# Performance work log

Hardware: AMD Instinct MI355X
Metric: run time of the kernel (lower is better)

Reference implementation:

```python
import jax, jax.numpy as jnp
from jax import lax
import numpy as np

# --- constants matching harris_laplace_detector_batch defaults ---
NUM_OCTAVES = 6
INITIAL_SIGMA = 1.4
HARRIS_K = 0.04
THRESHOLD = 0.01

SOBEL_X = jnp.array([[-1., 0., 1.], [-2., 0., 2.], [-1., 0., 1.]], jnp.float32)
SOBEL_Y = SOBEL_X.T
# OpenCV Laplacian kernel for ksize=3
LAP3 = jnp.array([[2., 0., 2.], [0., -8., 0.], [2., 0., 2.]], jnp.float32)


def _conv2d(x, k):
    """Cross-correlate x [N,H,W] with kernel k [kh,kw], reflect-101 padding (cv2 default)."""
    kh, kw = k.shape
    pt, pb = kh // 2, kh - 1 - kh // 2
    pl, pr = kw // 2, kw - 1 - kw // 2
    xp = jnp.pad(x, ((0, 0), (pt, pb), (pl, pr)), mode='reflect')
    out = lax.conv_general_dilated(xp[:, None], k[None, None], (1, 1), 'VALID')
    return out[:, 0]


def _gaussian_blur(x, sigma):
    """Separable Gaussian blur, truncated at ~3 sigma (static kernel size per octave)."""
    r = max(1, int(3.0 * sigma + 0.5))
    t = jnp.arange(-r, r + 1, dtype=jnp.float32)
    g = jnp.exp(-0.5 * (t / sigma) ** 2)
    g = g / g.sum()
    x = _conv2d(x, g[None, :])  # blur rows
    x = _conv2d(x, g[:, None])  # blur cols
    return x


def setup_inputs() -> dict:
    key = jax.random.key(0)
    images = jax.random.uniform(key, (16, 3, 512, 512), dtype=jnp.float32)
    return {"images": images}


def reference(images) -> jnp.ndarray:
    B, C, H, W = images.shape
    x = images.reshape(B * C, H, W)  # treat each channel independently, as the torch loop does

    # cv2.normalize(..., 0, 255, NORM_MINMAX) per channel (continuous analogue of uint8 cast)
    mn = x.min(axis=(1, 2), keepdims=True)
    mx = x.max(axis=(1, 2), keepdims=True)
    gray = (x - mn) / (mx - mn + 1e-12) * 255.0

    # Harris response: Sobel gradients (ksize=3), 2x2 unnormalized box sum (blockSize=2)
    Ix = _conv2d(gray, SOBEL_X)
    Iy = _conv2d(gray, SOBEL_Y)
    box = jnp.ones((2, 2), jnp.float32)
    Sxx = _conv2d(Ix * Ix, box)
    Syy = _conv2d(Iy * Iy, box)
    Sxy = _conv2d(Ix * Iy, box)
    R = Sxx * Syy - Sxy * Sxy - HARRIS_K * (Sxx + Syy) ** 2

    # cv2.dilate with default 3x3 kernel = 3x3 max filter
    Rd = lax.reduce_window(R, -jnp.inf, lax.max, (1, 3, 3), (1, 1, 1), 'SAME')
    mask = (Rd > THRESHOLD * Rd.max(axis=(1, 2), keepdims=True)).astype(jnp.float32)

    # multi-octave |scaled Laplacian| blurred at each sigma, max-combined
    lap_base = _conv2d(gray, LAP3)
    combined = jnp.zeros_like(gray)
    for octave in range(NUM_OCTAVES):
        sigma = INITIAL_SIGMA * (2.0 ** octave)
        lap = jnp.abs(_gaussian_blur(lap_base * sigma, sigma))
        combined = jnp.maximum(combined, mask * lap)

    # max over channels (the torch loop keeps running np.maximum across channels)
    corners = combined.reshape(B, C, H, W).max(axis=1, keepdims=True)  # [B,1,H,W]
    return corners
```

## Files before the change

### kernel.cpp

```cpp
#include <hip/hip_runtime.h>

#define W 512
#define NPX (512*512)
#define NCH 48
#define NBATCH 16

__device__ __forceinline__ int refl(int i) {
    int a = i < 0 ? -i : i;
    int b = 1022 - a;
    return a < b ? a : b;
}
__device__ __forceinline__ unsigned encf(float f) {
    unsigned u = __float_as_uint(f);
    return (u & 0x80000000u) ? ~u : (u | 0x80000000u);
}
__device__ __forceinline__ float decf(unsigned e) {
    unsigned u = (e & 0x80000000u) ? (e & 0x7FFFFFFFu) : ~e;
    return __uint_as_float(u);
}
__device__ __forceinline__ unsigned long long enc64(double d) {
    unsigned long long u = (unsigned long long)__double_as_longlong(d);
    return (u & 0x8000000000000000ULL) ? ~u : (u | 0x8000000000000000ULL);
}
__device__ __forceinline__ double dec64(unsigned long long e) {
    unsigned long long u = (e & 0x8000000000000000ULL) ? (e & 0x7FFFFFFFFFFFFFFFULL) : ~e;
    return __longlong_as_double((long long)u);
}

__global__ void initK(unsigned* minenc, unsigned* maxenc, unsigned long long* rmaxenc) {
    int t = threadIdx.x;
    if (t < NCH) { minenc[t] = 0xFFFFFFFFu; maxenc[t] = 0u; rmaxenc[t] = 0ULL; }
}

__global__ void gaussK(float* gw) {
    int o = blockIdx.x;
    const int rr[6] = {4, 8, 17, 34, 67, 134};
    int r = rr[o];
    float sigma = 1.4f * (float)(1 << o);
    int t = threadIdx.x;
    int n = 2*r + 1;
    float wv = 0.f;
    if (t < n) { float ft = (float)(t - r) / sigma; wv = expf(-0.5f * ft * ft); }
    __shared__ float red[512];
    red[t] = wv; __syncthreads();
    for (int s = 256; s > 0; s >>= 1) { if (t < s) red[t] += red[t + s]; __syncthreads(); }
    float sum = red[0];
    float* g = gw + o*288;
    if (t < 288) g[t] = (t < n) ? wv / sum : 0.f;
}

__global__ void minmaxK(const float4* __restrict__ x4, unsigned* minenc, unsigned* maxenc) {
    int ch = blockIdx.y, chunk = blockIdx.x, t = threadIdx.x;
    size_t base = (size_t)ch*(NPX/4) + (size_t)chunk*8192;
    float mn = 3.4e38f, mx = -3.4e38f;
    for (int i = t; i < 8192; i += 256) {
        float4 v = x4[base + i];
        mn = fminf(mn, fminf(fminf(v.x, v.y), fminf(v.z, v.w)));
        mx = fmaxf(mx, fmaxf(fmaxf(v.x, v.y), fmaxf(v.z, v.w)));
    }
    for (int o = 32; o; o >>= 1) { mn = fminf(mn, __shfl_down(mn, o)); mx = fmaxf(mx, __shfl_down(mx, o)); }
    __shared__ float smn[4], smx[4];
    if ((t & 63) == 0) { smn[t >> 6] = mn; smx[t >> 6] = mx; }
    __syncthreads();
    if (t == 0) {
        for (int i = 1; i < 4; i++) { mn = fminf(mn, smn[i]); mx = fmaxf(mx, smx[i]); }
        atomicMin(&minenc[ch], encf(mn));
        atomicMax(&maxenc[ch], encf(mx));
    }
}

__global__ void scaleK(const unsigned* minenc, const unsigned* maxenc, double* gsd) {
    int t = threadIdx.x;
    if (t >= NCH) return;
    double mn = (double)decf(minenc[t]), mx = (double)decf(maxenc[t]);
    gsd[t] = 255.0 / (mx - mn + 1e-12);
}

__global__ __launch_bounds__(256) void lapRK(const float* __restrict__ x, const double* __restrict__ gsd,
                      float* __restrict__ lap, double* __restrict__ Rb,
                      unsigned long long* __restrict__ rmaxenc) {
    __shared__ float in[36*36];
    __shared__ double Pxx[33*34], Pyy[33*34], Pxy[33*34];
    int ch = blockIdx.z;
    int px0 = blockIdx.x * 32, py0 = blockIdx.y * 32;
    const float* s = x + (size_t)ch*NPX;
    int t = threadIdx.x;
    for (int i = t; i < 36*36; i += 256) {
        int yy = i / 36, xx = i - yy*36;
        in[i] = s[(size_t)refl(py0 - 2 + yy)*W + refl(px0 - 2 + xx)];
    }
    __syncthreads();
    for (int i = t; i < 33*33; i += 256) {
        int ly = i / 33, lx = i - ly*33;
        const float* c = &in[(ly+1)*36 + (lx+1)];
        double v00 = c[-37], v01 = c[-36], v02 = c[-35];
        double v10 = c[-1],                v12 = c[1];
        double v20 = c[35],  v21 = c[36],  v22 = c[37];
        double ix = (v02 - v00) + 2.0*(v12 - v10) + (v22 - v20);
        double iy = (v20 - v00) + 2.0*(v21 - v01) + (v22 - v02);
        Pxx[ly*34+lx] = ix*ix; Pyy[ly*34+lx] = iy*iy; Pxy[ly*34+lx] = ix*iy;
    }
    __syncthreads();
    double sd = gsd[ch], s2 = sd*sd;
    int tx = t & 31, ty0 = (t >> 5) * 4;
    double m = -1e308;
    #pragma unroll
    for (int q = 0; q < 4; q++) {
        int ly = ty0 + q;
        int gy = py0 + ly, gx = px0 + tx;
        int ya = (gy ? gy-1 : 1) - py0 + 1;
        int yb = ly + 1;
        int xa = (gx ? gx-1 : 1) - px0 + 1;
        int xb = tx + 1;
        double Sxx = (Pxx[ya*34+xa] + Pxx[ya*34+xb]) + (Pxx[yb*34+xa] + Pxx[yb*34+xb]);
        double Syy = (Pyy[ya*34+xa] + Pyy[ya*34+xb]) + (Pyy[yb*34+xa] + Pyy[yb*34+xb]);
        double Sxy = (Pxy[ya*34+xa] + Pxy[ya*34+xb]) + (Pxy[yb*34+xa] + Pxy[yb*34+xb]);
        Sxx *= s2; Syy *= s2; Sxy *= s2;
        double tr = Sxx + Syy;
        double R = Sxx*Syy - Sxy*Sxy - 0.04*tr*tr;
        Rb[(size_t)ch*NPX + (size_t)gy*W + gx] = R;
        const float* c = &in[(ly+2)*36 + (tx+2)];
        double l = 2.0*((double)c[-37] + (double)c[-35] + (double)c[35] + (double)c[37]) - 8.0*(double)c[0];
        lap[(size_t)ch*NPX + (size_t)gy*W + gx] = (float)(sd * l);
        m = fmax(m, R);
    }
    for (int o = 32; o; o >>= 1) m = fmax(m, __shfl_down(m, o));
    __shared__ double sred[4];
    if ((t & 63) == 0) sred[t >> 6] = m;
    __syncthreads();
    if (t == 0) {
        for (int i = 1; i < 4; i++) m = fmax(m, sred[i]);
        atomicMax(&rmaxenc[ch], enc64(m));
    }
}

__global__ __launch_bounds__(256) void maskTK(const double* __restrict__ Rb,
                                              const unsigned long long* __restrict__ rmaxenc,
                                              unsigned char* __restrict__ maskb) {
    __shared__ int bt[34*34];
    int ch = blockIdx.z;
    int px0 = blockIdx.x*32, py0 = blockIdx.y*32;
    double thr = 0.01 * dec64(rmaxenc[ch]);
    const double* R = Rb + (size_t)ch*NPX;
    int t = threadIdx.x;
    for (int i = t; i < 34*34; i += 256) {
        int yy = i / 34, xx = i - yy*34;
        int gy = py0 - 1 + yy, gx = px0 - 1 + xx;
        int v = 0;
        if ((unsigned)gy < 512u && (unsigned)gx < 512u) v = (R[(size_t)gy*W + gx] > thr) ? 1 : 0;
        bt[i] = v;
    }
    __syncthreads();
    int tx = t & 31, ty0 = (t >> 5) * 4;
    #pragma unroll
    for (int q = 0; q < 4; q++) {
        int ly = ty0 + q;
        int c = (ly+1)*34 + tx + 1;
        int v = bt[c-35] | bt[c-34] | bt[c-33] | bt[c-1] | bt[c] | bt[c+1] | bt[c+33] | bt[c+34] | bt[c+35];
        maskb[(size_t)ch*NPX + (size_t)(py0+ly)*W + px0 + tx] = (unsigned char)v;
    }
}

__global__ __launch_bounds__(256) void rowblurK(const float* __restrict__ src, float* __restrict__ dst,
                                                const float* __restrict__ gwo, int r, int nc2) {
    __shared__ float ES[8][16][49];
    __shared__ float wl[272];
    int ch = blockIdx.y;
    int row0 = blockIdx.x * 8;
    int t = threadIdx.x;
    int lr = t >> 5, xi = t & 31;
    for (int i = t; i < 272; i += 256) wl[i] = gwo[i];
    const float* s = src + (size_t)ch*NPX + (size_t)(row0 + lr)*W;
    int n = W + 2*r;
    for (int j = xi; j < 784; j += 32) {
        float v = (j < n) ? s[refl(j - r)] : 0.f;
        ES[lr][j & 15][j >> 4] = v;
    }
    __syncthreads();
    float a[16];
    #pragma unroll
    for (int m = 0; m < 16; m++) a[m] = 0.f;
    for (int cc = 0; cc < nc2; ++cc) {
        float wv[16], f[31];
        #pragma unroll
        for (int i = 0; i < 16; i++) wv[i] = wl[16*cc + i];
        #pragma unroll
        for (int j = 0; j < 31; j++) f[j] = ES[lr][j & 15][xi + cc + (j >> 4)];
        #pragma unroll
        for (int m = 0; m < 16; m++) {
            #pragma unroll
            for (int i = 0; i < 16; i++) a[m] = fmaf(wv[i], f[m + i], a[m]);
        }
    }
    float4* d4 = (float4*)(dst + (size_t)ch*NPX + (size_t)(row0 + lr)*W + xi*16);
    d4[0] = make_float4(a[0],  a[1],  a[2],  a[3]);
    d4[1] = make_float4(a[4],  a[5],  a[6],  a[7]);
    d4[2] = make_float4(a[8],  a[9],  a[10], a[11]);
    d4[3] = make_float4(a[12], a[13], a[14], a[15]);
}

template<int RPT, int CHUNK>
__global__ __launch_bounds__(256, (RPT == 4) ? 4 : 2)
void colblurK(const float* __restrict__ T, const unsigned char* __restrict__ maskb,
              float* __restrict__ out, const float* __restrict__ gwo,
              int r, int nchunk, int rowsAlloc, float sigma, int write0) {
    extern __shared__ __align__(16) float tile[];
    float* wl = tile + rowsAlloc*36;
    const int BAND = RPT*32;
    int x0 = blockIdx.x * 32;
    int band0 = blockIdx.y * BAND;
    int b = blockIdx.z;
    int t = threadIdx.x;
    int cg = t & 7, rg = t >> 3;
    int j0 = rg * RPT;
    int rowsData = BAND + 2*r;
    for (int i = t; i < 288; i += 256) wl[i] = gwo[i];
    float4 vm[RPT];
    #pragma unroll
    for (int m = 0; m < RPT; m++) vm[m] = make_float4(0.f, 0.f, 0.f, 0.f);
    for (int c = 0; c < 3; ++c) {
        int ch = b*3 + c;
        __syncthreads();
        const float* src = T + (size_t)ch*NPX;
        for (int ly = rg; ly < rowsAlloc; ly += 32) {
            float4 v = make_float4(0.f, 0.f, 0.f, 0.f);
            if (ly < rowsData) v = *(const float4*)(src + (size_t)refl(band0 - r + ly)*W + x0 + 4*cg);
            *(float4*)(tile + ly*36 + 4*cg) = v;
        }
        __syncthreads();
        const unsigned char* mp = maskb + (size_t)ch*NPX + (size_t)(band0 + j0)*W + x0 + 4*cg;
        unsigned mk = 0;
        #pragma unroll
        for (int m = 0; m < RPT; m++) {
            uchar4 u = *(const uchar4*)(mp + (size_t)m*W);
            mk |= ((u.x ? 1u : 0u) | (u.y ? 2u : 0u) | (u.z ? 4u : 0u) | (u.w ? 8u : 0u)) << (4*m);
        }
        if (__any((int)(mk != 0))) {
            float4 a[RPT];
            #pragma unroll
            for (int m = 0; m < RPT; m++) a[m] = make_float4(0.f, 0.f, 0.f, 0.f);
            const float* tb = tile + j0*36 + 4*cg;
            for (int cc = 0; cc < nchunk; ++cc) {
                const float* tc = tb + CHUNK*cc*36;
                float4 f[RPT + CHUNK - 1];
                #pragma unroll
                for (int j = 0; j < RPT + CHUNK - 1; j++) f[j] = *(const float4*)(tc + j*36);
                float wv[CHUNK];
                #pragma unroll
                for (int q = 0; q < CHUNK/4; q++) {
                    float4 w4 = *(const float4*)(wl + CHUNK*cc + 4*q);
                    wv[4*q] = w4.x; wv[4*q+1] = w4.y; wv[4*q+2] = w4.z; wv[4*q+3] = w4.w;
                }
                #pragma unroll
                for (int m = 0; m < RPT; m++) {
                    #pragma unroll
                    for (int i = 0; i < CHUNK; i++) {
                        a[m].x = fmaf(wv[i], f[m+i].x, a[m].x);
                        a[m].y = fmaf(wv[i], f[m+i].y, a[m].y);
                        a[m].z = fmaf(wv[i], f[m+i].z, a[m].z);
                        a[m].w = fmaf(wv[i], f[m+i].w, a[m].w);
                    }
                }
            }
            #pragma unroll
            for (int m = 0; m < RPT; m++) {
                if (mk & (1u << (4*m+0))) vm[m].x = fmaxf(vm[m].x, sigma*fabsf(a[m].x));
                if (mk & (1u << (4*m+1))) vm[m].y = fmaxf(vm[m].y, sigma*fabsf(a[m].y));
                if (mk & (1u << (4*m+2))) vm[m].z = fmaxf(vm[m].z, sigma*fabsf(a[m].z));
                if (mk & (1u << (4*m+3))) vm[m].w = fmaxf(vm[m].w, sigma*fabsf(a[m].w));
            }
        }
    }
    float* ob = out + (size_t)b*NPX + (size_t)(band0 + j0)*W + x0 + 4*cg;
    #pragma unroll
    for (int m = 0; m < RPT; m++) {
        float4 v = vm[m];
        if (!write0) {
            float4 cur = *(const float4*)(ob + (size_t)m*W);
            v.x = fmaxf(v.x, cur.x); v.y = fmaxf(v.y, cur.y);
            v.z = fmaxf(v.z, cur.z); v.w = fmaxf(v.w, cur.w);
        }
        *(float4*)(ob + (size_t)m*W) = v;
    }
}

extern "C" void kernel_launch(void* const* d_in, const int* in_sizes, int n_in,
                              void* d_out, int out_size, void* d_ws, size_t ws_size,
                              hipStream_t stream) {
    const float* x = (const float*)d_in[0];
    float* out = (float*)d_out;
    char* w = (char*)d_ws;
    unsigned* minenc           = (unsigned*)(w + 1024);
    unsigned* maxenc           = (unsigned*)(w + 1280);
    unsigned long long* rmaxenc= (unsigned long long*)(w + 1536);
    double*  gsd               = (double*)(w + 256);
    float*   gw                = (float*)(w + 2048);
    float*   lap               = (float*)(w + 16384);
    double*  Rb                = (double*)(w + 16384 + 50331648);
    float*   T                 = (float*)Rb;
    unsigned char* maskb       = (unsigned char*)(w + 16384 + 50331648 + 100663296);

    initK<<<1, 64, 0, stream>>>(minenc, maxenc, rmaxenc);
    gaussK<<<6, 512, 0, stream>>>(gw);
    minmaxK<<<dim3(8, 48), 256, 0, stream>>>((const float4*)x, minenc, maxenc);
    scaleK<<<1, 64, 0, stream>>>(minenc, maxenc, gsd);
    lapRK<<<dim3(16, 16, 48), 256, 0, stream>>>(x, gsd, lap, Rb, rmaxenc);
    maskTK<<<dim3(16, 16, 48), 256, 0, stream>>>(Rb, rmaxenc, maskb);

    const int rr[6] = {4, 8, 17, 34, 67, 134};
    for (int o = 0; o < 6; ++o) {
        int r = rr[o];
        int nc16 = (2*r + 1 + 15) / 16;
        float sigma = 1.4f * (float)(1 << o);
        rowblurK<<<dim3(64, 48), 256, 0, stream>>>(lap, T, gw + o*288, r, nc16);
        if (o == 5) {
            int nc = nc16;
            int rowsAlloc = 256 + 16*nc;
            size_t lds = (size_t)(rowsAlloc*36 + 288) * 4;
            colblurK<8,16><<<dim3(16, 2, 16), 256, lds, stream>>>(T, maskb, out, gw + o*288, r, nc, rowsAlloc, sigma, 0);
        } else {
            int nc = (2*r + 1 + 7) / 8;
            int rowsAlloc = 128 + 8*nc;
            size_t lds = (size_t)(rowsAlloc*36 + 288) * 4;
            colblurK<4,8><<<dim3(16, 4, 16), 256, lds, stream>>>(T, maskb, out, gw + o*288, r, nc, rowsAlloc, sigma, o == 0 ? 1 : 0);
        }
    }
}
```

Baseline: 702.8 us.

## Skip blur work for mask-inactive rows and restructure Harris and column blur

Adds a per-channel row-activity bitmap built in the mask kernel and uses it to skip row-blur blocks and column-blur channels whose output is never selected by the mask. The Harris stage now computes Sobel gradients and the 2x2 box sum directly from registers instead of staging products in shared memory. The column blur becomes a single 8-row-per-thread variant with a sliding register window that reuses loaded rows across chunks. This adds atomics, extra launch arguments and larger LDS tiles, and the amount of work skipped depends on how sparse the mask is.

```diff
diff --git a/kernel.cpp b/kernel.cpp
--- a/kernel.cpp
+++ b/kernel.cpp
@@ -27,9 +27,11 @@
     return __longlong_as_double((long long)u);
 }
 
-__global__ void initK(unsigned* minenc, unsigned* maxenc, unsigned long long* rmaxenc) {
+__global__ void initK(unsigned* minenc, unsigned* maxenc, unsigned long long* rmaxenc,
+                      unsigned* rowact) {
     int t = threadIdx.x;
     if (t < NCH) { minenc[t] = 0xFFFFFFFFu; maxenc[t] = 0u; rmaxenc[t] = 0ULL; }
+    for (int i = t; i < NCH*16; i += 1024) rowact[i] = 0u;
 }
 
 __global__ void gaussK(float* gw) {
@@ -80,7 +82,6 @@
                       float* __restrict__ lap, double* __restrict__ Rb,
                       unsigned long long* __restrict__ rmaxenc) {
     __shared__ float in[36*36];
-    __shared__ double Pxx[33*34], Pyy[33*34], Pxy[33*34];
     int ch = blockIdx.z;
     int px0 = blockIdx.x * 32, py0 = blockIdx.y * 32;
     const float* s = x + (size_t)ch*NPX;
@@ -90,31 +91,42 @@
         in[i] = s[(size_t)refl(py0 - 2 + yy)*W + refl(px0 - 2 + xx)];
     }
     __syncthreads();
-    for (int i = t; i < 33*33; i += 256) {
-        int ly = i / 33, lx = i - ly*33;
-        const float* c = &in[(ly+1)*36 + (lx+1)];
-        double v00 = c[-37], v01 = c[-36], v02 = c[-35];
-        double v10 = c[-1],                v12 = c[1];
-        double v20 = c[35],  v21 = c[36],  v22 = c[37];
-        double ix = (v02 - v00) + 2.0*(v12 - v10) + (v22 - v20);
-        double iy = (v20 - v00) + 2.0*(v21 - v01) + (v22 - v02);
-        Pxx[ly*34+lx] = ix*ix; Pyy[ly*34+lx] = iy*iy; Pxy[ly*34+lx] = ix*iy;
-    }
-    __syncthreads();
     double sd = gsd[ch], s2 = sd*sd;
     int tx = t & 31, ty0 = (t >> 5) * 4;
+    int gx = px0 + tx;
+    int cb = gx ? tx : 1;
     double m = -1e308;
     #pragma unroll
     for (int q = 0; q < 4; q++) {
         int ly = ty0 + q;
-        int gy = py0 + ly, gx = px0 + tx;
-        int ya = (gy ? gy-1 : 1) - py0 + 1;
-        int yb = ly + 1;
-        int xa = (gx ? gx-1 : 1) - px0 + 1;
-        int xb = tx + 1;
-        double Sxx = (Pxx[ya*34+xa] + Pxx[ya*34+xb]) + (Pxx[yb*34+xa] + Pxx[yb*34+xb]);
-        double Syy = (Pyy[ya*34+xa] + Pyy[ya*34+xb]) + (Pyy[yb*34+xa] + Pyy[yb*34+xb]);
-        double Sxy = (Pxy[ya*34+xa] + Pxy[ya*34+xb]) + (Pxy[yb*34+xa] + Pxy[yb*34+xb]);
+        int gy = py0 + ly;
+        int rb = gy ? ly : 1;
+        double w[4][4];
+        #pragma unroll
+        for (int j = 0; j < 4; j++) {
+            const float* rp = &in[(rb + j)*36 + cb];
+            w[j][0] = (double)rp[0]; w[j][1] = (double)rp[1];
+            w[j][2] = (double)rp[2]; w[j][3] = (double)rp[3];
+        }
+        double cs1[4], cs2[4], rs[4][2];
+        #pragma unroll
+        for (int c2 = 0; c2 < 4; c2++) {
+            cs1[c2] = w[0][c2] + 2.0*w[1][c2] + w[2][c2];
+            cs2[c2] = w[1][c2] + 2.0*w[2][c2] + w[3][c2];
+        }
+        #pragma unroll
+        for (int j = 0; j < 4; j++) {
+            rs[j][0] = w[j][0] + 2.0*w[j][1] + w[j][2];
+            rs[j][1] = w[j][1] + 2.0*w[j][2] + w[j][3];
+        }
+        double Sxx = 0, Syy = 0, Sxy = 0;
+        {
+            double ix, iy;
+            ix = cs1[2]-cs1[0]; iy = rs[2][0]-rs[0][0]; Sxx += ix*ix; Syy += iy*iy; Sxy += ix*iy;
+            ix = cs1[3]-cs1[1]; iy = rs[2][1]-rs[0][1]; Sxx += ix*ix; Syy += iy*iy; Sxy += ix*iy;
+            ix = cs2[2]-cs2[0]; iy = rs[3][0]-rs[1][0]; Sxx += ix*ix; Syy += iy*iy; Sxy += ix*iy;
+            ix = cs2[3]-cs2[1]; iy = rs[3][1]-rs[1][1]; Sxx += ix*ix; Syy += iy*iy; Sxy += ix*iy;
+        }
         Sxx *= s2; Syy *= s2; Sxy *= s2;
         double tr = Sxx + Syy;
         double R = Sxx*Syy - Sxy*Sxy - 0.04*tr*tr;
@@ -136,13 +148,16 @@
 
 __global__ __launch_bounds__(256) void maskTK(const double* __restrict__ Rb,
                                               const unsigned long long* __restrict__ rmaxenc,
-                                              unsigned char* __restrict__ maskb) {
+                                              unsigned char* __restrict__ maskb,
+                                              unsigned* __restrict__ rowact) {
     __shared__ int bt[34*34];
+    __shared__ unsigned rw;
     int ch = blockIdx.z;
     int px0 = blockIdx.x*32, py0 = blockIdx.y*32;
     double thr = 0.01 * dec64(rmaxenc[ch]);
     const double* R = Rb + (size_t)ch*NPX;
     int t = threadIdx.x;
+    if (t == 0) rw = 0u;
     for (int i = t; i < 34*34; i += 256) {
         int yy = i / 34, xx = i - yy*34;
         int gy = py0 - 1 + yy, gx = px0 - 1 + xx;
@@ -158,16 +173,41 @@
         int c = (ly+1)*34 + tx + 1;
         int v = bt[c-35] | bt[c-34] | bt[c-33] | bt[c-1] | bt[c] | bt[c+1] | bt[c+33] | bt[c+34] | bt[c+35];
         maskb[(size_t)ch*NPX + (size_t)(py0+ly)*W + px0 + tx] = (unsigned char)v;
-    }
+        unsigned long long bal = __ballot(v != 0);
+        int lane = t & 63;
+        if (lane == 0 && (unsigned)bal) atomicOr(&rw, 1u << (ty0 + q));
+        if (lane == 32 && (unsigned)(bal >> 32)) atomicOr(&rw, 1u << (ty0 + q));
+    }
+    __syncthreads();
+    if (t == 0 && rw) atomicOr(&rowact[ch*16 + (py0 >> 5)], rw);
 }
 
 __global__ __launch_bounds__(256) void rowblurK(const float* __restrict__ src, float* __restrict__ dst,
-                                                const float* __restrict__ gwo, int r, int nc2) {
+                                                const float* __restrict__ gwo, int r, int nc2,
+                                                const unsigned* __restrict__ rowact) {
+    int ch = blockIdx.y;
+    int row0 = blockIdx.x * 8;
+    int t = threadIdx.x;
+    {
+        int lo = row0 - r - 7; if (lo < 0) lo = 0;
+        int hi = row0 + 7 + r; if (hi > 511) hi = 511;
+        int w0 = lo >> 5, w1 = hi >> 5;
+        int lane = t & 63;
+        unsigned any = 0;
+        if (lane <= w1 - w0) {
+            int wi = w0 + lane;
+            unsigned word = rowact[ch*16 + wi];
+            int b0 = wi*32;
+            int lo2 = lo > b0 ? lo - b0 : 0;
+            int hi2 = hi < b0 + 31 ? hi - b0 : 31;
+            unsigned mlo = ~0u << lo2;
+            unsigned mhi = (hi2 == 31) ? ~0u : ((1u << (hi2 + 1)) - 1u);
+            any = word & mlo & mhi;
+        }
+        if (!__any((int)(any != 0))) return;
+    }
     __shared__ float ES[8][16][49];
     __shared__ float wl[272];
-    int ch = blockIdx.y;
-    int row0 = blockIdx.x * 8;
-    int t = threadIdx.x;
     int lr = t >> 5, xi = t & 31;
     for (int i = t; i < 272; i += 256) wl[i] = gwo[i];
     const float* s = src + (size_t)ch*NPX + (size_t)(row0 + lr)*W;
@@ -199,28 +239,35 @@
     d4[3] = make_float4(a[12], a[13], a[14], a[15]);
 }
 
-template<int RPT, int CHUNK>
-__global__ __launch_bounds__(256, (RPT == 4) ? 4 : 2)
-void colblurK(const float* __restrict__ T, const unsigned char* __restrict__ maskb,
-              float* __restrict__ out, const float* __restrict__ gwo,
-              int r, int nchunk, int rowsAlloc, float sigma, int write0) {
+__global__ __launch_bounds__(256) void colblurK(const float* __restrict__ T, const unsigned char* __restrict__ maskb,
+                                                float* __restrict__ out, const float* __restrict__ gwo,
+                                                int r, int nchunk, int rowsAlloc, float sigma, int write0) {
     extern __shared__ __align__(16) float tile[];
     float* wl = tile + rowsAlloc*36;
-    const int BAND = RPT*32;
     int x0 = blockIdx.x * 32;
-    int band0 = blockIdx.y * BAND;
+    int band0 = blockIdx.y * 256;
     int b = blockIdx.z;
     int t = threadIdx.x;
     int cg = t & 7, rg = t >> 3;
-    int j0 = rg * RPT;
-    int rowsData = BAND + 2*r;
+    int j0 = rg * 8;
+    int rowsData = 256 + 2*r;
     for (int i = t; i < 288; i += 256) wl[i] = gwo[i];
-    float4 vm[RPT];
-    #pragma unroll
-    for (int m = 0; m < RPT; m++) vm[m] = make_float4(0.f, 0.f, 0.f, 0.f);
+    float4 vm[8];
+    #pragma unroll
+    for (int m = 0; m < 8; m++) vm[m] = make_float4(0.f, 0.f, 0.f, 0.f);
+    int anyAct = 0;
     for (int c = 0; c < 3; ++c) {
         int ch = b*3 + c;
-        __syncthreads();
+        const unsigned char* mp = maskb + (size_t)ch*NPX + (size_t)(band0 + j0)*W + x0 + 4*cg;
+        unsigned mk = 0;
+        #pragma unroll
+        for (int m = 0; m < 8; m++) {
+            uchar4 u = *(const uchar4*)(mp + (size_t)m*W);
+            mk |= ((u.x ? 1u : 0u) | (u.y ? 2u : 0u) | (u.z ? 4u : 0u) | (u.w ? 8u : 0u)) << (4*m);
+        }
+        int act = __syncthreads_or((int)(mk != 0));
+        if (!act) continue;
+        anyAct = 1;
         const float* src = T + (size_t)ch*NPX;
         for (int ly = rg; ly < rowsAlloc; ly += 32) {
             float4 v = make_float4(0.f, 0.f, 0.f, 0.f);
@@ -228,33 +275,31 @@
             *(float4*)(tile + ly*36 + 4*cg) = v;
         }
         __syncthreads();
-        const unsigned char* mp = maskb + (size_t)ch*NPX + (size_t)(band0 + j0)*W + x0 + 4*cg;
-        unsigned mk = 0;
-        #pragma unroll
-        for (int m = 0; m < RPT; m++) {
-            uchar4 u = *(const uchar4*)(mp + (size_t)m*W);
-            mk |= ((u.x ? 1u : 0u) | (u.y ? 2u : 0u) | (u.z ? 4u : 0u) | (u.w ? 8u : 0u)) << (4*m);
-        }
         if (__any((int)(mk != 0))) {
-            float4 a[RPT];
+            float4 a[8];
             #pragma unroll
-            for (int m = 0; m < RPT; m++) a[m] = make_float4(0.f, 0.f, 0.f, 0.f);
+            for (int m = 0; m < 8; m++) a[m] = make_float4(0.f, 0.f, 0.f, 0.f);
             const float* tb = tile + j0*36 + 4*cg;
+            float4 f[15];
+            #pragma unroll
+            for (int j = 0; j < 15; j++) f[j] = *(const float4*)(tb + j*36);
             for (int cc = 0; cc < nchunk; ++cc) {
-                const float* tc = tb + CHUNK*cc*36;
-                float4 f[RPT + CHUNK - 1];
+                if (cc) {
+                    #pragma unroll
+                    for (int j = 0; j < 7; j++) f[j] = f[j+8];
+                    #pragma unroll
+                    for (int j = 7; j < 15; j++) f[j] = *(const float4*)(tb + (8*cc + j)*36);
+                }
+                float wv[8];
                 #pragma unroll
-                for (int j = 0; j < RPT + CHUNK - 1; j++) f[j] = *(const float4*)(tc + j*36);
-                float wv[CHUNK];
-                #pragma unroll
-                for (int q = 0; q < CHUNK/4; q++) {
-                    float4 w4 = *(const float4*)(wl + CHUNK*cc + 4*q);
-                    wv[4*q] = w4.x; wv[4*q+1] = w4.y; wv[4*q+2] = w4.z; wv[4*q+3] = w4.w;
+                for (int qq = 0; qq < 2; qq++) {
+                    float4 w4 = *(const float4*)(wl + 8*cc + 4*qq);
+                    wv[4*qq] = w4.x; wv[4*qq+1] = w4.y; wv[4*qq+2] = w4.z; wv[4*qq+3] = w4.w;
                 }
                 #pragma unroll
-                for (int m = 0; m < RPT; m++) {
+                for (int m = 0; m < 8; m++) {
                     #pragma unroll
-                    for (int i = 0; i < CHUNK; i++) {
+                    for (int i = 0; i < 8; i++) {
                         a[m].x = fmaf(wv[i], f[m+i].x, a[m].x);
                         a[m].y = fmaf(wv[i], f[m+i].y, a[m].y);
                         a[m].z = fmaf(wv[i], f[m+i].z, a[m].z);
@@ -263,7 +308,7 @@
                 }
             }
             #pragma unroll
-            for (int m = 0; m < RPT; m++) {
+            for (int m = 0; m < 8; m++) {
                 if (mk & (1u << (4*m+0))) vm[m].x = fmaxf(vm[m].x, sigma*fabsf(a[m].x));
                 if (mk & (1u << (4*m+1))) vm[m].y = fmaxf(vm[m].y, sigma*fabsf(a[m].y));
                 if (mk & (1u << (4*m+2))) vm[m].z = fmaxf(vm[m].z, sigma*fabsf(a[m].z));
@@ -271,9 +316,10 @@
             }
         }
     }
+    if (!anyAct && !write0) return;
     float* ob = out + (size_t)b*NPX + (size_t)(band0 + j0)*W + x0 + 4*cg;
     #pragma unroll
-    for (int m = 0; m < RPT; m++) {
+    for (int m = 0; m < 8; m++) {
         float4 v = vm[m];
         if (!write0) {
             float4 cur = *(const float4*)(ob + (size_t)m*W);
@@ -295,34 +341,28 @@
     unsigned long long* rmaxenc= (unsigned long long*)(w + 1536);
     double*  gsd               = (double*)(w + 256);
     float*   gw                = (float*)(w + 2048);
+    unsigned* rowact           = (unsigned*)(w + 9216);
     float*   lap               = (float*)(w + 16384);
     double*  Rb                = (double*)(w + 16384 + 50331648);
     float*   T                 = (float*)Rb;
     unsigned char* maskb       = (unsigned char*)(w + 16384 + 50331648 + 100663296);
 
-    initK<<<1, 64, 0, stream>>>(minenc, maxenc, rmaxenc);
+    initK<<<1, 1024, 0, stream>>>(minenc, maxenc, rmaxenc, rowact);
     gaussK<<<6, 512, 0, stream>>>(gw);
     minmaxK<<<dim3(8, 48), 256, 0, stream>>>((const float4*)x, minenc, maxenc);
     scaleK<<<1, 64, 0, stream>>>(minenc, maxenc, gsd);
     lapRK<<<dim3(16, 16, 48), 256, 0, stream>>>(x, gsd, lap, Rb, rmaxenc);
-    maskTK<<<dim3(16, 16, 48), 256, 0, stream>>>(Rb, rmaxenc, maskb);
+    maskTK<<<dim3(16, 16, 48), 256, 0, stream>>>(Rb, rmaxenc, maskb, rowact);
 
     const int rr[6] = {4, 8, 17, 34, 67, 134};
     for (int o = 0; o < 6; ++o) {
         int r = rr[o];
         int nc16 = (2*r + 1 + 15) / 16;
+        int nc8  = (2*r + 1 + 7) / 8;
         float sigma = 1.4f * (float)(1 << o);
-        rowblurK<<<dim3(64, 48), 256, 0, stream>>>(lap, T, gw + o*288, r, nc16);
-        if (o == 5) {
-            int nc = nc16;
-            int rowsAlloc = 256 + 16*nc;
-            size_t lds = (size_t)(rowsAlloc*36 + 288) * 4;
-            colblurK<8,16><<<dim3(16, 2, 16), 256, lds, stream>>>(T, maskb, out, gw + o*288, r, nc, rowsAlloc, sigma, 0);
-        } else {
-            int nc = (2*r + 1 + 7) / 8;
-            int rowsAlloc = 128 + 8*nc;
-            size_t lds = (size_t)(rowsAlloc*36 + 288) * 4;
-            colblurK<4,8><<<dim3(16, 4, 16), 256, lds, stream>>>(T, maskb, out, gw + o*288, r, nc, rowsAlloc, sigma, o == 0 ? 1 : 0);
-        }
-    }
-}
+        rowblurK<<<dim3(64, 48), 256, 0, stream>>>(lap, T, gw + o*288, r, nc16, rowact);
+        int rowsAlloc = 256 + 8*nc8 + 8;
+        size_t lds = (size_t)(rowsAlloc*36 + 288) * 4;
+        colblurK<<<dim3(16, 2, 16), 256, lds, stream>>>(T, maskb, out, gw + o*288, r, nc8, rowsAlloc, sigma, o == 0 ? 1 : 0);
+    }
+}
```

New measurement: 730.4 us. 1.04x slower.
